# Kernel tuning notes

Measured on AMD Instinct MI355X. Metric: run time of the kernel, lower is better.

The kernel has to match this reference:

```python
import jax, jax.numpy as jnp
import numpy as np

DIM = 128
HEADS = 4
WS = 8  # window size
HEAD_DIM = DIM // HEADS
LOG100 = float(np.log(100.0))


def _cpb_constants(ws):
    # log-spaced relative coordinates table, shape [(2ws-1)^2, 2]
    rng = np.arange(-(ws - 1), ws, dtype=np.float32)
    table = np.stack(np.meshgrid(rng, rng, indexing='ij'), axis=-1)  # [2ws-1,2ws-1,2]
    table = table / (ws - 1)
    table = table * 8.0
    table = np.sign(table) * np.log2(np.abs(table) + 1.0) / np.log2(8.0)
    table = table.reshape(-1, 2)
    # relative position index, shape [ws^2, ws^2]
    coords = np.stack(np.meshgrid(np.arange(ws), np.arange(ws), indexing='ij'), axis=0).reshape(2, -1)
    rel = coords[:, :, None] - coords[:, None, :]  # [2, ws^2, ws^2]
    idx = (rel[0] + ws - 1) * (2 * ws - 1) + (rel[1] + ws - 1)
    return jnp.asarray(table), jnp.asarray(idx.astype(np.int32))


def setup_inputs() -> dict:
    key = jax.random.key(0)
    ks = jax.random.split(key, 10)
    B, H, W = 16, 128, 128
    nW = (H // WS) * (W // WS)
    return {
        'x': jax.random.normal(ks[0], (B, H, W, DIM), jnp.float32),
        'mask': jnp.zeros((nW, WS * WS, WS * WS), jnp.float32),
        'qkv_w': jax.random.normal(ks[1], (DIM, 3 * DIM), jnp.float32) * 0.02,
        'q_bias': jax.random.normal(ks[2], (DIM,), jnp.float32) * 0.02,
        'v_bias': jax.random.normal(ks[3], (DIM,), jnp.float32) * 0.02,
        'logit_scale': jnp.full((HEADS,), float(np.log(10.0)), jnp.float32),
        'cpb_w1': jax.random.normal(ks[4], (2, 512), jnp.float32) * 0.02,
        'cpb_b1': jax.random.normal(ks[5], (512,), jnp.float32) * 0.02,
        'cpb_w2': jax.random.normal(ks[6], (512, HEADS), jnp.float32) * 0.02,
        'proj_w': jax.random.normal(ks[7], (DIM, DIM), jnp.float32) * 0.02,
        'proj_b': jax.random.normal(ks[8], (DIM,), jnp.float32) * 0.02,
        'height': 128,
        'width': 128,
    }


def reference(x, mask, qkv_w, q_bias, v_bias, logit_scale, cpb_w1, cpb_b1, cpb_w2, proj_w, proj_b, height, width):
    B = x.shape[0]
    N = WS * WS
    wh, ww = height // WS, width // WS
    nW = wh * ww

    # QKV projection, K has no bias
    qkv_b = jnp.concatenate([q_bias, jnp.zeros_like(q_bias), v_bias])
    qkv = x @ qkv_w + qkv_b  # [B,H,W,3*DIM]

    # fused window partition -> [3, B*nW, heads, N, head_dim]
    qkv = qkv.reshape(B, wh, WS, ww, WS, 3, HEADS, HEAD_DIM)
    qkv = jnp.transpose(qkv, (5, 0, 1, 3, 6, 2, 4, 7)).reshape(3, B * nW, HEADS, N, HEAD_DIM)
    q, k, v = qkv[0], qkv[1], qkv[2]

    # cosine attention with clamped learnable temperature
    q = q / jnp.maximum(jnp.linalg.norm(q, axis=-1, keepdims=True), 1e-12)
    k = k / jnp.maximum(jnp.linalg.norm(k, axis=-1, keepdims=True), 1e-12)
    scale = jnp.exp(jnp.minimum(logit_scale, LOG100))  # [heads]
    attn = jnp.einsum('whqd,whkd->whqk', q, k) * scale[None, :, None, None]

    # continuous relative position bias via small MLP
    table, idx = _cpb_constants(WS)
    bias_tab = jax.nn.relu(table @ cpb_w1 + cpb_b1) @ cpb_w2  # [(2ws-1)^2, heads]
    bias = 16.0 * jax.nn.sigmoid(bias_tab[idx])  # [N, N, heads]
    attn = attn + jnp.transpose(bias, (2, 0, 1))[None]

    # shifted-window mask
    attn = attn.reshape(B, nW, HEADS, N, N) + mask[None, :, None, :, :]
    attn = jax.nn.softmax(attn.reshape(B * nW, HEADS, N, N), axis=-1)

    out = jnp.einsum('whqk,whkd->whqd', attn, v)  # [B*nW, heads, N, head_dim]

    # fused window reverse -> [B, H, W, DIM]
    out = out.reshape(B, wh, ww, HEADS, WS, WS, HEAD_DIM)
    out = jnp.transpose(out, (0, 1, 4, 2, 5, 3, 6)).reshape(B, height, width, DIM)

    return out @ proj_w + proj_b
```

## Files before the change

### kernel.cpp

```cpp
#include <hip/hip_runtime.h>

typedef unsigned short u16;
typedef __bf16 bf16x8 __attribute__((ext_vector_type(8)));
typedef float f32x4 __attribute__((ext_vector_type(4)));
typedef int i32x4 __attribute__((ext_vector_type(4)));
typedef i32x4 i32x4_a __attribute__((may_alias));
typedef bf16x8 bf16x8_a __attribute__((may_alias));

__device__ __forceinline__ float bf2f(u16 u) {
  union { unsigned int i; float f; } c;
  c.i = ((unsigned int)u) << 16;
  return c.f;
}
__device__ __forceinline__ u16 f2bf(float f) {
  union { float f; unsigned int i; } c;
  c.f = f;
  unsigned int r = c.i + 0x7fffu + ((c.i >> 16) & 1u);
  return (u16)(r >> 16);
}
__device__ __forceinline__ float gld(const void* p, int i, int isbf) {
  return isbf ? bf2f(((const u16*)p)[i]) : ((const float*)p)[i];
}
__device__ __forceinline__ int sw(int row, int col, int rs) {
  return row * rs + ((((col >> 3) ^ (row & 7)) << 3) | (col & 7));
}

#define WQKVT_OFF 0
#define PWT_OFF   98304
#define QKVB_OFF  131072
#define BIAS_OFF  132608
#define SCALE_OFF 198144
#define PB_OFF    198160
#define FLAG_OFF  198672

__global__ void swin_detect(const unsigned int* __restrict__ xw,
                            unsigned int* __restrict__ flag) {
  int t = threadIdx.x;
  int cnt = 0;
  for (int i = 0; i < 8; i++) {
    unsigned int w = xw[t * 8 + i];
    unsigned int lo = w & 0xffffu;
    unsigned int e = (lo >> 7) & 0xffu;
    if ((e >= 0x70u && e <= 0x82u) || lo == 0u) cnt++;
  }
  cnt += __shfl_xor(cnt, 1);
  cnt += __shfl_xor(cnt, 2);
  cnt += __shfl_xor(cnt, 4);
  cnt += __shfl_xor(cnt, 8);
  cnt += __shfl_xor(cnt, 16);
  cnt += __shfl_xor(cnt, 32);
  if (t == 0) *flag = (cnt >= 256) ? 1u : 0u;
}

__global__ void swin_setup(const void* __restrict__ qkv_w, const void* __restrict__ q_bias,
                           const void* __restrict__ v_bias, const void* __restrict__ ls,
                           const void* __restrict__ cpb_w1, const void* __restrict__ cpb_b1,
                           const void* __restrict__ cpb_w2, const void* __restrict__ proj_w,
                           const void* __restrict__ proj_b, char* __restrict__ ws) {
  const int b = blockIdx.x, t = threadIdx.x;
  const int isbf = (int)*(const unsigned int*)(ws + FLAG_OFF);
  u16* wqkvT = (u16*)(ws + WQKVT_OFF);
  u16* pwT = (u16*)(ws + PWT_OFF);
  float* qkvb = (float*)(ws + QKVB_OFF);
  float* bias16 = (float*)(ws + BIAS_OFF);
  float* scalef = (float*)(ws + SCALE_OFF);
  float* pbf = (float*)(ws + PB_OFF);

  if (b < 128) {
    for (int c = t; c < 384; c += 256)
      wqkvT[c * 128 + b] = f2bf(gld(qkv_w, b * 384 + c, isbf));
  } else if (b < 256) {
    int r = b - 128;
    if (t < 128) pwT[t * 128 + r] = f2bf(gld(proj_w, r * 128 + t, isbf));
  } else if (b == 256) {
    for (int o = t; o < 384; o += 256) {
      float v = 0.f;
      if (o < 128) v = gld(q_bias, o, isbf);
      else if (o >= 256) v = gld(v_bias, o - 256, isbf);
      qkvb[o] = v;
    }
    if (t < 128) pbf[t] = gld(proj_b, t, isbf);
    if (t < 4) scalef[t] = expf(fminf(gld(ls, t, isbf), 4.60517019f));
  } else {
    __shared__ float w1[1024];
    __shared__ float b1[512];
    __shared__ float w2[2048];
    __shared__ float tab[225][4];
    for (int i = t; i < 1024; i += 256) w1[i] = gld(cpb_w1, i, isbf);
    for (int i = t; i < 512; i += 256) b1[i] = gld(cpb_b1, i, isbf);
    for (int i = t; i < 2048; i += 256) w2[i] = gld(cpb_w2, i, isbf);
    __syncthreads();
    if (t < 225) {
      int i = t / 15, j = t % 15;
      float c0, c1;
      {
        float tt = ((float)(i - 7) / 7.0f) * 8.0f;
        float s = (tt > 0.f) ? 1.f : ((tt < 0.f) ? -1.f : 0.f);
        c0 = s * log2f(fabsf(tt) + 1.f) / 3.0f;
      }
      {
        float tt = ((float)(j - 7) / 7.0f) * 8.0f;
        float s = (tt > 0.f) ? 1.f : ((tt < 0.f) ? -1.f : 0.f);
        c1 = s * log2f(fabsf(tt) + 1.f) / 3.0f;
      }
      float acc[4] = {0.f, 0.f, 0.f, 0.f};
      for (int jj = 0; jj < 512; jj++) {
        float h = fmaxf(c0 * w1[jj] + c1 * w1[512 + jj] + b1[jj], 0.f);
        #pragma unroll
        for (int hh = 0; hh < 4; hh++) acc[hh] += h * w2[jj * 4 + hh];
      }
      #pragma unroll
      for (int hh = 0; hh < 4; hh++) tab[t][hh] = acc[hh];
    }
    __syncthreads();
    for (int e = t; e < 4 * 64 * 64; e += 256) {
      int h = e >> 12, q = (e >> 6) & 63, kk = e & 63;
      int dr = (q >> 3) - (kk >> 3) + 7;
      int dc = (q & 7) - (kk & 7) + 7;
      float v = tab[dr * 15 + dc][h];
      bias16[e] = 16.f / (1.f + expf(-v));
    }
  }
}

#define X_OFF 0
#define Q_OFF 8192
#define K_OFF 16384
#define AO_OFF 16384
#define VT_OFF 24576
#define P_OFF 0

__global__ __launch_bounds__(512, 4) void swin_main(
    const void* __restrict__ x, const void* __restrict__ mask,
    const char* __restrict__ ws, void* __restrict__ out) {
  __shared__ __align__(16) u16 lds[32768];
  const f32x4 fz = {0.f, 0.f, 0.f, 0.f};

  const u16* wqkvT = (const u16*)(ws + WQKVT_OFF);
  const u16* pwT = (const u16*)(ws + PWT_OFF);
  const float* qkvb = (const float*)(ws + QKVB_OFF);
  const float* bias16 = (const float*)(ws + BIAS_OFF);
  const float* scalef = (const float*)(ws + SCALE_OFF);
  const float* pbf = (const float*)(ws + PB_OFF);
  const int isbf = (int)*(const unsigned int*)(ws + FLAG_OFF);

  const int tid = threadIdx.x;
  const int wid = tid >> 6;
  const int lane = tid & 63;
  const int ln16 = lane & 15;
  const int lq = lane >> 4;
  const int q8 = lq << 3;
  const int mg = wid >> 2;
  const int sub = wid & 3;

  const int wi = blockIdx.x;
  const int b = wi >> 8;
  const int rem = wi & 255;
  const int wy = rem >> 4, wx = rem & 15;
  const int xbase = ((b * 128 + wy * 8) * 128 + wx * 8) * 128;

  if (isbf) {
    const u16* xb = (const u16*)x;
    #pragma unroll
    for (int rep = 0; rep < 2; rep++) {
      int ch = tid + rep * 512;
      int token = ch >> 4, dch = ch & 15;
      int r = token >> 3, c = token & 7;
      i32x4 v = *(const i32x4_a*)(xb + xbase + r * 16384 + c * 128 + dch * 8);
      *(i32x4_a*)(lds + sw(token, dch * 8, 128)) = v;
    }
  } else {
    const float* xf = (const float*)x;
    #pragma unroll
    for (int rep = 0; rep < 2; rep++) {
      int ch = tid + rep * 512;
      int token = ch >> 4, dch = ch & 15;
      int r = token >> 3, c = token & 7;
      const float* src = xf + xbase + r * 16384 + c * 128 + dch * 8;
      union { i32x4 v2[2]; float f[8]; } in;
      in.v2[0] = *(const i32x4_a*)(src);
      in.v2[1] = *(const i32x4_a*)(src + 4);
      union { u16 u[8]; i32x4 v; } o;
      #pragma unroll
      for (int d = 0; d < 8; d++) o.u[d] = f2bf(in.f[d]);
      *(i32x4_a*)(lds + sw(token, dch * 8, 128)) = o.v;
    }
  }
  __syncthreads();

  f32x4 acc1[2][6];
  #pragma unroll
  for (int mt = 0; mt < 2; mt++)
    #pragma unroll
    for (int nt = 0; nt < 6; nt++) acc1[mt][nt] = fz;

  #pragma unroll
  for (int ks = 0; ks < 4; ks++) {
    bf16x8 a0 = *(const bf16x8_a*)(lds + X_OFF + sw(32 * mg + ln16, 32 * ks + q8, 128));
    bf16x8 a1 = *(const bf16x8_a*)(lds + X_OFF + sw(32 * mg + 16 + ln16, 32 * ks + q8, 128));
    bf16x8 bb[6];
    #pragma unroll
    for (int nt = 0; nt < 6; nt++)
      bb[nt] = *(const bf16x8_a*)(wqkvT + (96 * sub + 16 * nt + ln16) * 128 + 32 * ks + q8);
    #pragma unroll
    for (int nt = 0; nt < 6; nt++) {
      acc1[0][nt] = __builtin_amdgcn_mfma_f32_16x16x32_bf16(a0, bb[nt], acc1[0][nt], 0, 0, 0);
      acc1[1][nt] = __builtin_amdgcn_mfma_f32_16x16x32_bf16(a1, bb[nt], acc1[1][nt], 0, 0, 0);
    }
  }
  #pragma unroll
  for (int nt = 0; nt < 6; nt++) {
    float bv = qkvb[96 * sub + 16 * nt + ln16];
    #pragma unroll
    for (int mt = 0; mt < 2; mt++)
      #pragma unroll
      for (int r = 0; r < 4; r++) acc1[mt][nt][r] += bv;
  }
  #pragma unroll
  for (int ci = 0; ci < 3; ci++) {
    int n0 = 96 * sub + 32 * ci;
    int type = n0 >> 7;
    int head = (n0 & 127) >> 5;
    int nt0 = 2 * ci, nt1 = nt0 + 1;
    if (type < 2) {
      int base = (type == 0) ? Q_OFF : K_OFF;
      #pragma unroll
      for (int mt = 0; mt < 2; mt++)
        #pragma unroll
        for (int r = 0; r < 4; r++) {
          float x0 = acc1[mt][nt0][r], x1 = acc1[mt][nt1][r];
          float ss = x0 * x0 + x1 * x1;
          ss += __shfl_xor(ss, 1);
          ss += __shfl_xor(ss, 2);
          ss += __shfl_xor(ss, 4);
          ss += __shfl_xor(ss, 8);
          float inv = 1.0f / fmaxf(sqrtf(ss), 1e-12f);
          int row = 32 * mg + 16 * mt + 4 * lq + r;
          lds[base + sw(row, head * 32 + ln16, 128)] = f2bf(x0 * inv);
          lds[base + sw(row, head * 32 + 16 + ln16, 128)] = f2bf(x1 * inv);
        }
    } else {
      #pragma unroll
      for (int mt = 0; mt < 2; mt++)
        #pragma unroll
        for (int r = 0; r < 4; r++) {
          int row = 32 * mg + 16 * mt + 4 * lq + r;
          lds[VT_OFF + sw(head * 32 + ln16, row, 64)] = f2bf(acc1[mt][nt0][r]);
          lds[VT_OFF + sw(head * 32 + 16 + ln16, row, 64)] = f2bf(acc1[mt][nt1][r]);
        }
    }
  }
  __syncthreads();

  const int h = sub;
  const float scale = scalef[h];
  bf16x8 qf[2], kf[4];
  #pragma unroll
  for (int mt = 0; mt < 2; mt++)
    qf[mt] = *(const bf16x8_a*)(lds + Q_OFF + sw(32 * mg + 16 * mt + ln16, h * 32 + q8, 128));
  #pragma unroll
  for (int nt = 0; nt < 4; nt++)
    kf[nt] = *(const bf16x8_a*)(lds + K_OFF + sw(16 * nt + ln16, h * 32 + q8, 128));
  f32x4 S[2][4];
  #pragma unroll
  for (int mt = 0; mt < 2; mt++)
    #pragma unroll
    for (int nt = 0; nt < 4; nt++)
      S[mt][nt] = __builtin_amdgcn_mfma_f32_16x16x32_bf16(qf[mt], kf[nt], fz, 0, 0, 0);

  const float* brow = bias16 + h * 4096;
  const u16* mk16 = (const u16*)mask;
  const float* mkf = (const float*)mask;
  #pragma unroll
  for (int mt = 0; mt < 2; mt++)
    #pragma unroll
    for (int r = 0; r < 4; r++) {
      int row = 32 * mg + 16 * mt + 4 * lq + r;
      #pragma unroll
      for (int nt = 0; nt < 4; nt++) {
        int col = 16 * nt + ln16;
        int mi = rem * 4096 + row * 64 + col;
        float mval = isbf ? bf2f(mk16[mi]) : mkf[mi];
        S[mt][nt][r] = S[mt][nt][r] * scale + brow[row * 64 + col] + mval;
      }
    }
  #pragma unroll
  for (int mt = 0; mt < 2; mt++)
    #pragma unroll
    for (int r = 0; r < 4; r++) {
      float m = fmaxf(fmaxf(S[mt][0][r], S[mt][1][r]), fmaxf(S[mt][2][r], S[mt][3][r]));
      m = fmaxf(m, __shfl_xor(m, 1));
      m = fmaxf(m, __shfl_xor(m, 2));
      m = fmaxf(m, __shfl_xor(m, 4));
      m = fmaxf(m, __shfl_xor(m, 8));
      float sum = 0.f;
      #pragma unroll
      for (int nt = 0; nt < 4; nt++) {
        float p = __expf(S[mt][nt][r] - m);
        S[mt][nt][r] = p;
        sum += p;
      }
      sum += __shfl_xor(sum, 1);
      sum += __shfl_xor(sum, 2);
      sum += __shfl_xor(sum, 4);
      sum += __shfl_xor(sum, 8);
      float inv = 1.0f / sum;
      #pragma unroll
      for (int nt = 0; nt < 4; nt++) S[mt][nt][r] *= inv;
    }
  __syncthreads();

  #pragma unroll
  for (int mt = 0; mt < 2; mt++)
    #pragma unroll
    for (int nt = 0; nt < 4; nt++)
      #pragma unroll
      for (int r = 0; r < 4; r++) {
        int row = 32 * mg + 16 * mt + 4 * lq + r;
        lds[P_OFF + sw(row, h * 64 + 16 * nt + ln16, 256)] = f2bf(S[mt][nt][r]);
      }
  __syncthreads();
  f32x4 O[2][2];
  O[0][0] = fz; O[0][1] = fz; O[1][0] = fz; O[1][1] = fz;
  #pragma unroll
  for (int ks = 0; ks < 2; ks++) {
    bf16x8 pf[2], vf[2];
    #pragma unroll
    for (int mt = 0; mt < 2; mt++)
      pf[mt] = *(const bf16x8_a*)(lds + P_OFF + sw(32 * mg + 16 * mt + ln16, h * 64 + 32 * ks + q8, 256));
    #pragma unroll
    for (int nt = 0; nt < 2; nt++)
      vf[nt] = *(const bf16x8_a*)(lds + VT_OFF + sw(h * 32 + 16 * nt + ln16, 32 * ks + q8, 64));
    #pragma unroll
    for (int mt = 0; mt < 2; mt++)
      #pragma unroll
      for (int nt = 0; nt < 2; nt++)
        O[mt][nt] = __builtin_amdgcn_mfma_f32_16x16x32_bf16(pf[mt], vf[nt], O[mt][nt], 0, 0, 0);
  }
  #pragma unroll
  for (int mt = 0; mt < 2; mt++)
    #pragma unroll
    for (int nt = 0; nt < 2; nt++)
      #pragma unroll
      for (int r = 0; r < 4; r++) {
        int row = 32 * mg + 16 * mt + 4 * lq + r;
        lds[AO_OFF + sw(row, h * 32 + 16 * nt + ln16, 128)] = f2bf(O[mt][nt][r]);
      }
  __syncthreads();

  f32x4 acc3[2][2];
  acc3[0][0] = fz; acc3[0][1] = fz; acc3[1][0] = fz; acc3[1][1] = fz;
  #pragma unroll
  for (int ks = 0; ks < 4; ks++) {
    bf16x8 a0 = *(const bf16x8_a*)(lds + AO_OFF + sw(32 * mg + ln16, 32 * ks + q8, 128));
    bf16x8 a1 = *(const bf16x8_a*)(lds + AO_OFF + sw(32 * mg + 16 + ln16, 32 * ks + q8, 128));
    bf16x8 b0 = *(const bf16x8_a*)(pwT + (32 * sub + ln16) * 128 + 32 * ks + q8);
    bf16x8 b1 = *(const bf16x8_a*)(pwT + (32 * sub + 16 + ln16) * 128 + 32 * ks + q8);
    acc3[0][0] = __builtin_amdgcn_mfma_f32_16x16x32_bf16(a0, b0, acc3[0][0], 0, 0, 0);
    acc3[0][1] = __builtin_amdgcn_mfma_f32_16x16x32_bf16(a0, b1, acc3[0][1], 0, 0, 0);
    acc3[1][0] = __builtin_amdgcn_mfma_f32_16x16x32_bf16(a1, b0, acc3[1][0], 0, 0, 0);
    acc3[1][1] = __builtin_amdgcn_mfma_f32_16x16x32_bf16(a1, b1, acc3[1][1], 0, 0, 0);
  }
  float pb0 = pbf[32 * sub + ln16];
  float pb1 = pbf[32 * sub + 16 + ln16];
  if (isbf) {
    u16* ob = (u16*)out;
    #pragma unroll
    for (int mt = 0; mt < 2; mt++)
      #pragma unroll
      for (int r = 0; r < 4; r++) {
        int row = 32 * mg + 16 * mt + 4 * lq + r;
        int o = xbase + (row >> 3) * 16384 + (row & 7) * 128 + 32 * sub;
        ob[o + ln16] = f2bf(acc3[mt][0][r] + pb0);
        ob[o + 16 + ln16] = f2bf(acc3[mt][1][r] + pb1);
      }
  } else {
    float* of = (float*)out;
    #pragma unroll
    for (int mt = 0; mt < 2; mt++)
      #pragma unroll
      for (int r = 0; r < 4; r++) {
        int row = 32 * mg + 16 * mt + 4 * lq + r;
        int o = xbase + (row >> 3) * 16384 + (row & 7) * 128 + 32 * sub;
        of[o + ln16] = acc3[mt][0][r] + pb0;
        of[o + 16 + ln16] = acc3[mt][1][r] + pb1;
      }
  }
}

extern "C" void kernel_launch(void* const* d_in, const int* in_sizes, int n_in,
                              void* d_out, int out_size, void* d_ws, size_t ws_size,
                              hipStream_t stream) {
  const void* x      = d_in[0];
  const void* mask   = d_in[1];
  const void* qkv_w  = d_in[2];
  const void* q_bias = d_in[3];
  const void* v_bias = d_in[4];
  const void* ls     = d_in[5];
  const void* cpb_w1 = d_in[6];
  const void* cpb_b1 = d_in[7];
  const void* cpb_w2 = d_in[8];
  const void* proj_w = d_in[9];
  const void* proj_b = d_in[10];
  const int B = in_sizes[0] / (128 * 128 * 128);

  char* ws = (char*)d_ws;
  swin_detect<<<1, 64, 0, stream>>>((const unsigned int*)x,
                                    (unsigned int*)(ws + FLAG_OFF));
  swin_setup<<<258, 256, 0, stream>>>(qkv_w, q_bias, v_bias, ls, cpb_w1, cpb_b1,
                                      cpb_w2, proj_w, proj_b, ws);
  swin_main<<<B * 256, 512, 0, stream>>>(x, mask, ws, d_out);
}
```

Baseline: 431.9 us.

## Shrink LDS footprint via buffer aliasing, fold biases and scale into MFMA accumulators

Reworks the shared-memory layout so Q, K, V^T, P and the attention output alias the X staging buffer. This cuts LDS from 64KB to 48KB per block and raises launch bounds to allow 6 blocks per CU. The QKV bias, relative-position bias plus mask, and projection bias are now preloaded into the MFMA accumulators instead of added afterwards. The logit scale is folded into the Q normalization, and the float-to-bf16 conversion uses the hardware cast. Reusing the buffers needs extra __syncthreads barriers, and the higher occupancy target may force register spills.

```diff
diff --git a/kernel.cpp b/kernel.cpp
--- a/kernel.cpp
+++ b/kernel.cpp
@@ -13,10 +13,9 @@
   return c.f;
 }
 __device__ __forceinline__ u16 f2bf(float f) {
-  union { float f; unsigned int i; } c;
-  c.f = f;
-  unsigned int r = c.i + 0x7fffu + ((c.i >> 16) & 1u);
-  return (u16)(r >> 16);
+  union { __bf16 h; u16 u; } c;
+  c.h = (__bf16)f;
+  return c.u;
 }
 __device__ __forceinline__ float gld(const void* p, int i, int isbf) {
   return isbf ? bf2f(((const u16*)p)[i]) : ((const float*)p)[i];
@@ -124,16 +123,16 @@
 }
 
 #define X_OFF 0
-#define Q_OFF 8192
-#define K_OFF 16384
-#define AO_OFF 16384
-#define VT_OFF 24576
+#define Q_OFF 0
+#define K_OFF 8192
+#define VT_OFF 16384
 #define P_OFF 0
-
-__global__ __launch_bounds__(512, 4) void swin_main(
+#define AO_OFF 0
+
+__global__ __launch_bounds__(512, 6) void swin_main(
     const void* __restrict__ x, const void* __restrict__ mask,
     const char* __restrict__ ws, void* __restrict__ out) {
-  __shared__ __align__(16) u16 lds[32768];
+  __shared__ __align__(16) u16 lds[24576];
   const f32x4 fz = {0.f, 0.f, 0.f, 0.f};
 
   const u16* wqkvT = (const u16*)(ws + WQKVT_OFF);
@@ -167,7 +166,7 @@
       int token = ch >> 4, dch = ch & 15;
       int r = token >> 3, c = token & 7;
       i32x4 v = *(const i32x4_a*)(xb + xbase + r * 16384 + c * 128 + dch * 8);
-      *(i32x4_a*)(lds + sw(token, dch * 8, 128)) = v;
+      *(i32x4_a*)(lds + X_OFF + sw(token, dch * 8, 128)) = v;
     }
   } else {
     const float* xf = (const float*)x;
@@ -183,16 +182,19 @@
       union { u16 u[8]; i32x4 v; } o;
       #pragma unroll
       for (int d = 0; d < 8; d++) o.u[d] = f2bf(in.f[d]);
-      *(i32x4_a*)(lds + sw(token, dch * 8, 128)) = o.v;
+      *(i32x4_a*)(lds + X_OFF + sw(token, dch * 8, 128)) = o.v;
     }
   }
   __syncthreads();
 
   f32x4 acc1[2][6];
   #pragma unroll
-  for (int mt = 0; mt < 2; mt++)
-    #pragma unroll
-    for (int nt = 0; nt < 6; nt++) acc1[mt][nt] = fz;
+  for (int nt = 0; nt < 6; nt++) {
+    float bv = qkvb[96 * sub + 16 * nt + ln16];
+    f32x4 ci = {bv, bv, bv, bv};
+    acc1[0][nt] = ci;
+    acc1[1][nt] = ci;
+  }
 
   #pragma unroll
   for (int ks = 0; ks < 4; ks++) {
@@ -208,14 +210,8 @@
       acc1[1][nt] = __builtin_amdgcn_mfma_f32_16x16x32_bf16(a1, bb[nt], acc1[1][nt], 0, 0, 0);
     }
   }
-  #pragma unroll
-  for (int nt = 0; nt < 6; nt++) {
-    float bv = qkvb[96 * sub + 16 * nt + ln16];
-    #pragma unroll
-    for (int mt = 0; mt < 2; mt++)
-      #pragma unroll
-      for (int r = 0; r < 4; r++) acc1[mt][nt][r] += bv;
-  }
+  __syncthreads();
+
   #pragma unroll
   for (int ci = 0; ci < 3; ci++) {
     int n0 = 96 * sub + 32 * ci;
@@ -224,6 +220,7 @@
     int nt0 = 2 * ci, nt1 = nt0 + 1;
     if (type < 2) {
       int base = (type == 0) ? Q_OFF : K_OFF;
+      float sh = (type == 0) ? scalef[head] : 1.0f;
       #pragma unroll
       for (int mt = 0; mt < 2; mt++)
         #pragma unroll
@@ -234,7 +231,7 @@
           ss += __shfl_xor(ss, 2);
           ss += __shfl_xor(ss, 4);
           ss += __shfl_xor(ss, 8);
-          float inv = 1.0f / fmaxf(sqrtf(ss), 1e-12f);
+          float inv = sh / fmaxf(sqrtf(ss), 1e-12f);
           int row = 32 * mg + 16 * mt + 4 * lq + r;
           lds[base + sw(row, head * 32 + ln16, 128)] = f2bf(x0 * inv);
           lds[base + sw(row, head * 32 + 16 + ln16, 128)] = f2bf(x1 * inv);
@@ -253,7 +250,6 @@
   __syncthreads();
 
   const int h = sub;
-  const float scale = scalef[h];
   bf16x8 qf[2], kf[4];
   #pragma unroll
   for (int mt = 0; mt < 2; mt++)
@@ -261,29 +257,29 @@
   #pragma unroll
   for (int nt = 0; nt < 4; nt++)
     kf[nt] = *(const bf16x8_a*)(lds + K_OFF + sw(16 * nt + ln16, h * 32 + q8, 128));
-  f32x4 S[2][4];
-  #pragma unroll
-  for (int mt = 0; mt < 2; mt++)
-    #pragma unroll
-    for (int nt = 0; nt < 4; nt++)
-      S[mt][nt] = __builtin_amdgcn_mfma_f32_16x16x32_bf16(qf[mt], kf[nt], fz, 0, 0, 0);
 
   const float* brow = bias16 + h * 4096;
   const u16* mk16 = (const u16*)mask;
   const float* mkf = (const float*)mask;
-  #pragma unroll
-  for (int mt = 0; mt < 2; mt++)
-    #pragma unroll
-    for (int r = 0; r < 4; r++) {
-      int row = 32 * mg + 16 * mt + 4 * lq + r;
-      #pragma unroll
-      for (int nt = 0; nt < 4; nt++) {
+  f32x4 S[2][4];
+  #pragma unroll
+  for (int mt = 0; mt < 2; mt++)
+    #pragma unroll
+    for (int nt = 0; nt < 4; nt++)
+      #pragma unroll
+      for (int r = 0; r < 4; r++) {
+        int row = 32 * mg + 16 * mt + 4 * lq + r;
         int col = 16 * nt + ln16;
-        int mi = rem * 4096 + row * 64 + col;
-        float mval = isbf ? bf2f(mk16[mi]) : mkf[mi];
-        S[mt][nt][r] = S[mt][nt][r] * scale + brow[row * 64 + col] + mval;
-      }
-    }
+        int bi = row * 64 + col;
+        float mval = isbf ? bf2f(mk16[rem * 4096 + bi]) : mkf[rem * 4096 + bi];
+        S[mt][nt][r] = brow[bi] + mval;
+      }
+  #pragma unroll
+  for (int mt = 0; mt < 2; mt++)
+    #pragma unroll
+    for (int nt = 0; nt < 4; nt++)
+      S[mt][nt] = __builtin_amdgcn_mfma_f32_16x16x32_bf16(qf[mt], kf[nt], S[mt][nt], 0, 0, 0);
+
   #pragma unroll
   for (int mt = 0; mt < 2; mt++)
     #pragma unroll
@@ -337,6 +333,7 @@
       for (int nt = 0; nt < 2; nt++)
         O[mt][nt] = __builtin_amdgcn_mfma_f32_16x16x32_bf16(pf[mt], vf[nt], O[mt][nt], 0, 0, 0);
   }
+  __syncthreads();
   #pragma unroll
   for (int mt = 0; mt < 2; mt++)
     #pragma unroll
@@ -348,8 +345,14 @@
       }
   __syncthreads();
 
+  float pb0 = pbf[32 * sub + ln16];
+  float pb1 = pbf[32 * sub + 16 + ln16];
   f32x4 acc3[2][2];
-  acc3[0][0] = fz; acc3[0][1] = fz; acc3[1][0] = fz; acc3[1][1] = fz;
+  {
+    f32x4 c0 = {pb0, pb0, pb0, pb0};
+    f32x4 c1 = {pb1, pb1, pb1, pb1};
+    acc3[0][0] = c0; acc3[0][1] = c1; acc3[1][0] = c0; acc3[1][1] = c1;
+  }
   #pragma unroll
   for (int ks = 0; ks < 4; ks++) {
     bf16x8 a0 = *(const bf16x8_a*)(lds + AO_OFF + sw(32 * mg + ln16, 32 * ks + q8, 128));
@@ -361,8 +364,6 @@
     acc3[1][0] = __builtin_amdgcn_mfma_f32_16x16x32_bf16(a1, b0, acc3[1][0], 0, 0, 0);
     acc3[1][1] = __builtin_amdgcn_mfma_f32_16x16x32_bf16(a1, b1, acc3[1][1], 0, 0, 0);
   }
-  float pb0 = pbf[32 * sub + ln16];
-  float pb1 = pbf[32 * sub + 16 + ln16];
   if (isbf) {
     u16* ob = (u16*)out;
     #pragma unroll
@@ -371,8 +372,8 @@
       for (int r = 0; r < 4; r++) {
         int row = 32 * mg + 16 * mt + 4 * lq + r;
         int o = xbase + (row >> 3) * 16384 + (row & 7) * 128 + 32 * sub;
-        ob[o + ln16] = f2bf(acc3[mt][0][r] + pb0);
-        ob[o + 16 + ln16] = f2bf(acc3[mt][1][r] + pb1);
+        ob[o + ln16] = f2bf(acc3[mt][0][r]);
+        ob[o + 16 + ln16] = f2bf(acc3[mt][1][r]);
       }
   } else {
     float* of = (float*)out;
@@ -382,8 +383,8 @@
       for (int r = 0; r < 4; r++) {
         int row = 32 * mg + 16 * mt + 4 * lq + r;
         int o = xbase + (row >> 3) * 16384 + (row & 7) * 128 + 32 * sub;
-        of[o + ln16] = acc3[mt][0][r] + pb0;
-        of[o + 16 + ln16] = acc3[mt][1][r] + pb1;
+        of[o + ln16] = acc3[mt][0][r];
+        of[o + 16 + ln16] = acc3[mt][1][r];
       }
   }
 }
```

New measurement: 536.5 us. 1.24x slower.
